# Kernel tuning notes

Measured on AMD Instinct MI355X. Metric: run time of the kernel, lower is better.

Reference implementation:

```python
import jax, jax.numpy as jnp
import numpy as np
from jax.scipy.linalg import solve_triangular

B, T, D = 2, 8192, 1024
HEAD_DIM = 128
H = D // HEAD_DIM  # 8 heads
C = 64             # chunk size (hard-coded in the torch module)


def setup_inputs() -> dict:
    key = jax.random.key(0)
    k0, k1, k2, k3 = jax.random.split(key, 4)
    scale = 0.02
    return {
        "out": jax.random.normal(k0, (B, T, D), jnp.float32),
        "W_write": jax.random.normal(k1, (D, D), jnp.float32) * scale,   # proj_write.weight (out,in)
        "W_read": jax.random.normal(k2, (D, D), jnp.float32) * scale,    # proj_read.weight
        "W_beta": jax.random.normal(k3, (H, D), jnp.float32) * scale,    # proj_beta.weight
        "decay": jnp.full((H,), 4.6, jnp.float32),                        # decay parameter
    }


def reference(out, W_write, W_read, W_beta, decay):
    Bs, Ts, Ds = out.shape
    d = HEAD_DIM
    Hn = Ds // d
    x = out.astype(jnp.float32)

    # keys: L2-normalized per head (F.normalize, eps=1e-12)
    k = x.reshape(Bs, Ts, Hn, d)
    k = k / jnp.maximum(jnp.linalg.norm(k, axis=-1, keepdims=True), 1e-12)
    k = k.transpose(0, 2, 1, 3)                                   # (B,H,T,d)
    v = (x @ W_write.T).reshape(Bs, Ts, Hn, d).transpose(0, 2, 1, 3)
    beta = jax.nn.sigmoid(x @ W_beta.T).transpose(0, 2, 1)[..., None]  # (B,H,T,1)
    v = v * beta
    k_beta = k * beta

    pad = (-Ts) % C
    if pad:
        pw = ((0, 0), (0, 0), (0, pad), (0, 0))
        k, v, k_beta = (jnp.pad(a, pw) for a in (k, v, k_beta))
    Tp = k.shape[2]
    N = Tp // C

    log_gamma = jnp.log(jax.nn.sigmoid(decay))                     # (H,)
    pos = jnp.arange(C, dtype=jnp.float32)
    cum_decay = (pos + 1.0)[None, :] * log_gamma[:, None]          # (H,C)
    Ldiff = cum_decay[:, :, None] - cum_decay[:, None, :]
    L = jnp.tril(jnp.exp(jnp.tril(Ldiff)))                         # (H,C,C)
    decay_exp = jnp.exp(cum_decay)[None, :, None, :, None]         # (1,H,1,C,1)
    chunk_total_decay = jnp.exp(cum_decay[:, -1])[None, :, None, None]  # (1,H,1,1)
    dw = jnp.exp(cum_decay[:, -1:] - cum_decay)[None, :, :, None]  # (1,H,C,1)
    de = jnp.exp(cum_decay)[None, :, :, None]                      # (1,H,C,1)

    k = k.reshape(Bs, Hn, N, C, d)
    v = v.reshape(Bs, Hn, N, C, d)
    k_beta = k_beta.reshape(Bs, Hn, N, C, d)

    # UT transform: original loop computes A = (I - A0)^{-1} with A0 strictly lower
    A0 = jnp.tril(-(jnp.einsum('bhnid,bhnjd->bhnij', k_beta, k) * L[None, :, None]), -1)
    eye = jnp.eye(C, dtype=jnp.float32)
    M = eye - A0                                                    # unit-diag lower triangular
    A = solve_triangular(M, jnp.broadcast_to(eye, M.shape), lower=True, unit_diagonal=True)

    v = A @ v
    k_cumdecay = A @ (k_beta * decay_exp)

    # inter-chunk sequential recurrence over N chunks
    kc = k.transpose(2, 0, 1, 3, 4)            # (N,B,H,C,d)
    vc = v.transpose(2, 0, 1, 3, 4)
    kcd = k_cumdecay.transpose(2, 0, 1, 3, 4)

    def step(S, inp):
        k_i, v_i, kcd_i = inp                  # (B,H,C,d)
        attn = jnp.tril(jnp.einsum('bhid,bhjd->bhij', k_i, k_i) * L[None])
        v_new = v_i - kcd_i @ S
        o_i = (k_i * de) @ S + attn @ v_new
        S_new = chunk_total_decay * S + jnp.einsum('bhcd,bhce->bhde', k_i * dw, v_new)
        return S_new, o_i

    S0 = jnp.zeros((Bs, Hn, d, d), jnp.float32)
    _, o = jax.lax.scan(step, S0, (kc, vc, kcd))  # o: (N,B,H,C,d)

    o = o.transpose(1, 2, 0, 3, 4).reshape(Bs, Hn, Tp, d)
    o = o.transpose(0, 2, 1, 3).reshape(Bs, Tp, Ds)[:, :Ts]
    return out + (o @ W_read.T).astype(out.dtype)
```

## Files before the change

### kernel.cpp

```cpp
#include <hip/hip_runtime.h>
#include <stdint.h>

#define DEV static __device__ __forceinline__

typedef float          f32x4  __attribute__((ext_vector_type(4)));
typedef short          bf16x8 __attribute__((ext_vector_type(8)));
typedef unsigned short u16x4  __attribute__((ext_vector_type(4)));
typedef unsigned short u16x8  __attribute__((ext_vector_type(8)));

#define B_   2
#define T_   8192
#define D_   1024
#define H_   8
#define HD_  128
#define N_   128

DEV float dot4(const float4& a, const float4& b) {
    return a.x * b.x + a.y * b.y + a.z * b.z + a.w * b.w;
}
DEV unsigned short f2bf(float f) {
    union { float f; unsigned u; } v; v.f = f;
    unsigned r = (v.u + 0x7fffu + ((v.u >> 16) & 1u)) >> 16;
    return (unsigned short)r;
}
DEV float bf2f(unsigned short u) {
    union { unsigned u; float f; } v; v.u = ((unsigned)u) << 16;
    return v.f;
}
DEV void cvt4(const float4 v, u16x4* h, u16x4* l) {
    const float* p = (const float*)&v;
    #pragma unroll
    for (int i = 0; i < 4; ++i) {
        unsigned short hv = f2bf(p[i]);
        (*h)[i] = hv;
        (*l)[i] = f2bf(p[i] - bf2f(hv));
    }
}
DEV void bar_lgkm() {
    asm volatile("s_waitcnt lgkmcnt(0)" ::: "memory");
    __builtin_amdgcn_s_barrier();
}
DEV float4* r512(char* base, int r, int u) {
    return (float4*)(base + (r << 9) + ((u << 4) ^ ((r & 7) << 4)));
}
DEV float ld_sk(char* base, int c, int dk) {
    return *(float*)(base + (c << 9) + ((((dk >> 2) << 4) ^ ((c & 7) << 4)) + ((dk & 3) << 2)));
}

__launch_bounds__(256)
__global__ void prep_kernel(const float* __restrict__ X, const float* __restrict__ Wb,
                            unsigned short* __restrict__ khi, unsigned short* __restrict__ klo,
                            float* __restrict__ beta) {
    int bt = blockIdx.x;
    int b = bt >> 13, t = bt & 8191;
    __shared__ float xrow[D_];
    const float* xp = X + (size_t)bt * D_;
    for (int i = threadIdx.x; i < D_; i += 256) xrow[i] = xp[i];
    __syncthreads();
    int w = threadIdx.x >> 6, lane = threadIdx.x & 63;
    for (int h = w; h < H_; h += 4) {
        const float* xh = xrow + h * HD_;
        float a0 = xh[lane], a1 = xh[lane + 64];
        float s = a0 * a0 + a1 * a1;
        #pragma unroll
        for (int off = 32; off > 0; off >>= 1) s += __shfl_xor(s, off);
        float rn = 1.0f / fmaxf(sqrtf(s), 1e-12f);
        const float* wbh = Wb + (size_t)h * D_;
        float bs = 0.f;
        for (int i = lane; i < D_; i += 64) bs += xrow[i] * wbh[i];
        #pragma unroll
        for (int off = 32; off > 0; off >>= 1) bs += __shfl_xor(bs, off);
        float bet = 1.0f / (1.0f + expf(-bs));
        size_t kbase = ((size_t)(b * H_ + h) * T_ + t) * HD_;
        float x0 = a0 * rn, x1 = a1 * rn;
        unsigned short h0 = f2bf(x0), h1 = f2bf(x1);
        khi[kbase + lane]      = h0;
        khi[kbase + lane + 64] = h1;
        klo[kbase + lane]      = f2bf(x0 - bf2f(h0));
        klo[kbase + lane + 64] = f2bf(x1 - bf2f(h1));
        if (lane == 0) beta[(size_t)(b * H_ + h) * T_ + t] = bet;
    }
}

__launch_bounds__(256, 2)
__global__ void vproj_kernel(const float* __restrict__ X, const float* __restrict__ W,
                             const float* __restrict__ beta, float* __restrict__ vb) {
    extern __shared__ char gs[];
    char* AH = gs;
    char* AL = gs + 16384;
    char* BH = gs + 32768;
    char* BL = gs + 49152;
    int bm = blockIdx.x, bn = blockIdx.y;
    int tid = threadIdx.x;
    int w = tid >> 6, lr = tid & 15, lk = (tid & 63) >> 4;
    int wm = w >> 1, wn = w & 1;

    f32x4 acc[4][4];
    #pragma unroll
    for (int i = 0; i < 4; ++i)
        #pragma unroll
        for (int j = 0; j < 4; ++j) acc[i][j] = (f32x4){0.f, 0.f, 0.f, 0.f};

    for (int kt = 0; kt < 16; ++kt) {
        __syncthreads();
        #pragma unroll
        for (int q = 0; q < 8; ++q) {
            int f = tid + q * 256;
            int row = f >> 4, kq = f & 15;
            float4 av = *(const float4*)(X + (size_t)(bm * 128 + row) * D_ + kt * 64 + kq * 4);
            float4 bv = *(const float4*)(W + (size_t)(bn * 128 + row) * D_ + kt * 64 + kq * 4);
            u16x4 ah, al, bh, bl;
            cvt4(av, &ah, &al);
            cvt4(bv, &bh, &bl);
            int off = row * 128 + ((((kq >> 1) ^ (row & 7))) << 4) + ((kq & 1) << 3);
            *(u16x4*)(AH + off) = ah; *(u16x4*)(AL + off) = al;
            *(u16x4*)(BH + off) = bh; *(u16x4*)(BL + off) = bl;
        }
        __syncthreads();
        #pragma unroll
        for (int ks = 0; ks < 2; ++ks) {
            bf16x8 aH[4], aL[4], bH[4], bL[4];
            #pragma unroll
            for (int mt = 0; mt < 4; ++mt) {
                int row = wm * 64 + mt * 16 + lr;
                int off = row * 128 + (((ks * 4 + lk) ^ (row & 7)) << 4);
                aH[mt] = *(const bf16x8*)(AH + off);
                aL[mt] = *(const bf16x8*)(AL + off);
            }
            #pragma unroll
            for (int nt = 0; nt < 4; ++nt) {
                int row = wn * 64 + nt * 16 + lr;
                int off = row * 128 + (((ks * 4 + lk) ^ (row & 7)) << 4);
                bH[nt] = *(const bf16x8*)(BH + off);
                bL[nt] = *(const bf16x8*)(BL + off);
            }
            #pragma unroll
            for (int mt = 0; mt < 4; ++mt)
                #pragma unroll
                for (int nt = 0; nt < 4; ++nt) {
                    acc[mt][nt] = __builtin_amdgcn_mfma_f32_16x16x32_bf16(aH[mt], bH[nt], acc[mt][nt], 0, 0, 0);
                    acc[mt][nt] = __builtin_amdgcn_mfma_f32_16x16x32_bf16(aH[mt], bL[nt], acc[mt][nt], 0, 0, 0);
                    acc[mt][nt] = __builtin_amdgcn_mfma_f32_16x16x32_bf16(aL[mt], bH[nt], acc[mt][nt], 0, 0, 0);
                }
        }
    }
    #pragma unroll
    for (int mt = 0; mt < 4; ++mt)
        #pragma unroll
        for (int r = 0; r < 4; ++r) {
            int m = bm * 128 + wm * 64 + mt * 16 + lk * 4 + r;
            int b = m >> 13, t = m & 8191;
            float bet = beta[(size_t)(b * H_ + bn) * T_ + t];
            size_t ob = ((size_t)(b * H_ + bn) * T_ + t) * HD_;
            #pragma unroll
            for (int nt = 0; nt < 4; ++nt)
                vb[ob + wn * 64 + nt * 16 + lr] = acc[mt][nt][r] * bet;
        }
}

__launch_bounds__(256, 2)
__global__ void chunk_kernel(const unsigned short* __restrict__ khi,
                             const unsigned short* __restrict__ klo,
                             float* __restrict__ vb,
                             const float* __restrict__ beta_g,
                             const float* __restrict__ decay,
                             unsigned short* __restrict__ attn_g,
                             unsigned short* __restrict__ kcdhi_g,
                             unsigned short* __restrict__ kcdlo_g,
                             unsigned short* __restrict__ kdwh_g,
                             unsigned short* __restrict__ kdwl_g) {
    extern __shared__ char cs[];
    char*  sk = cs;
    float* sa = (float*)(cs + 32768);
    float* sm = (float*)(cs + 49152);
    __shared__ float sb[64];
    __shared__ float swgt[64];

    int cid = blockIdx.x;
    int bh = cid >> 7, cn = cid & 127;
    int h = bh & 7;
    int tid = threadIdx.x;
    float dec = decay[h];
    float sg = 1.0f / (1.0f + expf(-dec));
    float lg = logf(sg);
    size_t base = (size_t)cid * 8192;

    #pragma unroll
    for (int lq = 0; lq < 4; ++lq) {
        int f = tid + lq * 256;
        int c = f >> 4, u0 = (f & 15) << 1;
        u16x8 hh = *(const u16x8*)(khi + base + (size_t)f * 8);
        u16x8 ll = *(const u16x8*)(klo + base + (size_t)f * 8);
        float4 v0 = {bf2f(hh[0]) + bf2f(ll[0]), bf2f(hh[1]) + bf2f(ll[1]),
                     bf2f(hh[2]) + bf2f(ll[2]), bf2f(hh[3]) + bf2f(ll[3])};
        float4 v1 = {bf2f(hh[4]) + bf2f(ll[4]), bf2f(hh[5]) + bf2f(ll[5]),
                     bf2f(hh[6]) + bf2f(ll[6]), bf2f(hh[7]) + bf2f(ll[7])};
        *r512(sk, c, u0)     = v0;
        *r512(sk, c, u0 + 1) = v1;
    }
    if (tid < 64) {
        float bv = beta_g[(size_t)bh * T_ + cn * 64 + tid];
        sb[tid] = bv;
        swgt[tid] = bv * expf((float)(tid + 1) * lg);
    }
    __syncthreads();

    int bi = tid >> 4, bj = tid & 15;
    float dacc[4][4] = {};
    for (int u = 0; u < 32; ++u) {
        float4 ka[4], kc[4];
        #pragma unroll
        for (int i = 0; i < 4; ++i) ka[i] = *r512(sk, bi * 4 + i, u);
        #pragma unroll
        for (int j = 0; j < 4; ++j) kc[j] = *r512(sk, bj + 16 * j, u);
        #pragma unroll
        for (int i = 0; i < 4; ++i)
            #pragma unroll
            for (int j = 0; j < 4; ++j)
                dacc[i][j] += dot4(ka[i], kc[j]);
    }
    size_t abase = (size_t)cid * 4096;
    #pragma unroll
    for (int i = 0; i < 4; ++i) {
        int gi = bi * 4 + i;
        #pragma unroll
        for (int j = 0; j < 4; ++j) {
            int gj = bj + 16 * j;
            float dv = dacc[i][j];
            float dfac = expf((float)(gi - gj) * lg);
            attn_g[abase + (size_t)gi * 64 + gj] = (gi >= gj) ? f2bf(dv * dfac) : (unsigned short)0;
            sm[gi * 64 + gj] = (gj < gi) ? sb[gi] * dv * dfac : ((gi == gj) ? 1.f : 0.f);
        }
    }
    __syncthreads();

    if (tid < 64) {
        int j = tid;
        for (int i = 0; i < j; ++i) sa[i * 64 + j] = 0.f;
        sa[j * 64 + j] = 1.f;
        for (int i = j + 1; i < 64; ++i) {
            float s = 0.f;
            for (int p = j; p < i; ++p) s += sm[i * 64 + p] * sa[p * 64 + j];
            sa[i * 64 + j] = -s;
        }
    }
    __syncthreads();

    int ti = tid >> 4, te = tid & 15;
    {
        float ko[4][8] = {};
        for (int p = 0; p < 64; ++p) {
            float w = swgt[p];
            float4 k0 = *r512(sk, p, te * 2);
            float4 k1 = *r512(sk, p, te * 2 + 1);
            float kv[8] = {k0.x, k0.y, k0.z, k0.w, k1.x, k1.y, k1.z, k1.w};
            float a0 = sa[(ti * 4 + 0) * 64 + p] * w;
            float a1 = sa[(ti * 4 + 1) * 64 + p] * w;
            float a2 = sa[(ti * 4 + 2) * 64 + p] * w;
            float a3 = sa[(ti * 4 + 3) * 64 + p] * w;
            #pragma unroll
            for (int e = 0; e < 8; ++e) {
                ko[0][e] = fmaf(a0, kv[e], ko[0][e]);
                ko[1][e] = fmaf(a1, kv[e], ko[1][e]);
                ko[2][e] = fmaf(a2, kv[e], ko[2][e]);
                ko[3][e] = fmaf(a3, kv[e], ko[3][e]);
            }
        }
        #pragma unroll
        for (int i = 0; i < 4; ++i) {
            u16x8 hh, ll;
            #pragma unroll
            for (int e = 0; e < 8; ++e) {
                float t = -ko[i][e];
                unsigned short hv = f2bf(t);
                hh[e] = hv;
                ll[e] = f2bf(t - bf2f(hv));
            }
            size_t off = base + (size_t)(ti * 4 + i) * 128 + te * 8;
            *(u16x8*)(kcdhi_g + off) = hh;
            *(u16x8*)(kcdlo_g + off) = ll;
        }
    }

    {
        int dk = tid >> 1, ch = (tid & 1) * 32;
        #pragma unroll
        for (int q = 0; q < 4; ++q) {
            u16x8 th, tl;
            #pragma unroll
            for (int j = 0; j < 8; ++j) {
                int c = ch + q * 8 + j;
                float kv = ld_sk(sk, c, dk) * expf((float)(63 - c) * lg);
                unsigned short hv = f2bf(kv);
                th[j] = hv;
                tl[j] = f2bf(kv - bf2f(hv));
            }
            size_t off = base + (size_t)dk * 64 + ch + q * 8;
            *(u16x8*)(kdwh_g + off) = th;
            if (kdwl_g) *(u16x8*)(kdwl_g + off) = tl;
        }
    }
    __syncthreads();

    #pragma unroll
    for (int lq = 0; lq < 8; ++lq) {
        int f = tid + lq * 256;
        int r = f >> 5, u = f & 31;
        *r512(sk, r, u) = ((const float4*)(vb + base))[f];
    }
    __syncthreads();

    {
        float vo[4][8] = {};
        for (int p = 0; p < 64; ++p) {
            float4 v0 = *r512(sk, p, te * 2);
            float4 v1 = *r512(sk, p, te * 2 + 1);
            float vv[8] = {v0.x, v0.y, v0.z, v0.w, v1.x, v1.y, v1.z, v1.w};
            float a0 = sa[(ti * 4 + 0) * 64 + p];
            float a1 = sa[(ti * 4 + 1) * 64 + p];
            float a2 = sa[(ti * 4 + 2) * 64 + p];
            float a3 = sa[(ti * 4 + 3) * 64 + p];
            #pragma unroll
            for (int e = 0; e < 8; ++e) {
                vo[0][e] = fmaf(a0, vv[e], vo[0][e]);
                vo[1][e] = fmaf(a1, vv[e], vo[1][e]);
                vo[2][e] = fmaf(a2, vv[e], vo[2][e]);
                vo[3][e] = fmaf(a3, vv[e], vo[3][e]);
            }
        }
        #pragma unroll
        for (int i = 0; i < 4; ++i) {
            float4 lo = {vo[i][0], vo[i][1], vo[i][2], vo[i][3]};
            float4 hi = {vo[i][4], vo[i][5], vo[i][6], vo[i][7]};
            size_t off = base + (size_t)(ti * 4 + i) * 128 + te * 8;
            *(float4*)(vb + off)     = lo;
            *(float4*)(vb + off + 4) = hi;
        }
    }
}

__launch_bounds__(512, 1)
__global__ void scan_kernel(const unsigned short* __restrict__ khi,
                            const unsigned short* __restrict__ klo,
                            float* __restrict__ vb,
                            const unsigned short* __restrict__ kcdh,
                            const unsigned short* __restrict__ kcdl,
                            const unsigned short* __restrict__ att,
                            const unsigned short* __restrict__ kdwh,
                            const unsigned short* __restrict__ kdwl,
                            const float* __restrict__ decay) {
    __shared__ char SH[4096];
    __shared__ char SL[4096];
    __shared__ char VH[2048];
    __shared__ char VL[2048];

    int bid = blockIdx.x;
    int bh = ((bid >> 6) << 3) + (bid & 7);
    int strip = (bid >> 3) & 7;
    int e0 = strip * 16;
    int tid = threadIdx.x;
    int w = tid >> 6, l = tid & 63, lr = l & 15, lk = l >> 4;
    int grp = w >> 2, cw = w & 3;
    float dec = decay[bh & 7];
    float sg = 1.0f / (1.0f + expf(-dec));
    float lg = logf(sg);
    float g64 = expf(64.f * lg);
    float dev4[4];
    #pragma unroll
    for (int r = 0; r < 4; ++r)
        dev4[r] = expf((float)(cw * 16 + lk * 4 + r + 1) * lg);
    const bool haveLo = (kdwl != nullptr);

    f32x4 Sacc = (f32x4){0.f, 0.f, 0.f, 0.f};

    bf16x8 fH[4], fL[4];
    bf16x8 atA[2];
    f32x4 vnA;

    {
        size_t nb = (size_t)bh * N_ * 8192;
        size_t na = (size_t)bh * N_ * 4096;
        if (grp == 0) {
            #pragma unroll
            for (int ks = 0; ks < 4; ++ks) {
                size_t off = nb + (size_t)(cw * 16 + lr) * 128 + ks * 32 + lk * 8;
                fH[ks] = *(const bf16x8*)(kcdh + off);
                fL[ks] = *(const bf16x8*)(kcdl + off);
            }
            #pragma unroll
            for (int r = 0; r < 4; ++r)
                vnA[r] = vb[nb + (size_t)(cw * 16 + lk * 4 + r) * 128 + e0 + lr];
        } else {
            #pragma unroll
            for (int ks = 0; ks < 4; ++ks) {
                size_t off = nb + (size_t)(cw * 16 + lr) * 128 + ks * 32 + lk * 8;
                fH[ks] = *(const bf16x8*)(khi + off);
                fL[ks] = *(const bf16x8*)(klo + off);
            }
            #pragma unroll
            for (int ks2 = 0; ks2 < 2; ++ks2)
                atA[ks2] = *(const bf16x8*)(att + na + (size_t)(cw * 16 + lr) * 64 + ks2 * 32 + lk * 8);
        }
    }

    for (int cn = 0; cn < N_; ++cn) {
        size_t cb8 = ((size_t)bh * N_ + cn) * 8192;

        bf16x8 tH[2], tL[2];
        #pragma unroll
        for (int ks2 = 0; ks2 < 2; ++ks2) {
            size_t off = cb8 + (size_t)(w * 16 + lr) * 64 + ks2 * 32 + lk * 8;
            tH[ks2] = *(const bf16x8*)(kdwh + off);
            if (haveLo) tL[ks2] = *(const bf16x8*)(kdwl + off);
        }

        {
            u16x4 h4, l4;
            #pragma unroll
            for (int r = 0; r < 4; ++r) {
                unsigned short hv = f2bf(Sacc[r]);
                h4[r] = hv;
                l4[r] = f2bf(Sacc[r] - bf2f(hv));
            }
            int unit = 2 * w + (lk >> 1);
            int off = lr * 256 + ((unit ^ (lr & 7)) << 4) + ((lk & 1) << 3);
            *(u16x4*)(SH + off) = h4;
            *(u16x4*)(SL + off) = l4;
        }
        bar_lgkm();

        bf16x8 BH[4], BL[4];
        #pragma unroll
        for (int ks = 0; ks < 4; ++ks) {
            int off = lr * 256 + (((ks * 4 + lk) ^ (lr & 7)) << 4);
            BH[ks] = *(const bf16x8*)(SH + off);
            BL[ks] = *(const bf16x8*)(SL + off);
        }
        f32x4 acc1, acc2;
        if (grp == 0) {
            acc1 = vnA; acc2 = (f32x4){0.f, 0.f, 0.f, 0.f};
            __builtin_amdgcn_s_setprio(1);
            #pragma unroll
            for (int ks = 0; ks < 2; ++ks) {
                acc1 = __builtin_amdgcn_mfma_f32_16x16x32_bf16(fH[ks], BH[ks], acc1, 0, 0, 0);
                acc2 = __builtin_amdgcn_mfma_f32_16x16x32_bf16(fH[ks+2], BH[ks+2], acc2, 0, 0, 0);
                acc1 = __builtin_amdgcn_mfma_f32_16x16x32_bf16(fH[ks], BL[ks], acc1, 0, 0, 0);
                acc2 = __builtin_amdgcn_mfma_f32_16x16x32_bf16(fH[ks+2], BL[ks+2], acc2, 0, 0, 0);
                acc1 = __builtin_amdgcn_mfma_f32_16x16x32_bf16(fL[ks], BH[ks], acc1, 0, 0, 0);
                acc2 = __builtin_amdgcn_mfma_f32_16x16x32_bf16(fL[ks+2], BH[ks+2], acc2, 0, 0, 0);
            }
            __builtin_amdgcn_s_setprio(0);
            u16x4 h4, l4;
            #pragma unroll
            for (int r = 0; r < 4; ++r) {
                float vv = acc1[r] + acc2[r];
                unsigned short hv = f2bf(vv);
                h4[r] = hv; l4[r] = f2bf(vv - bf2f(hv));
            }
            int cu = 2 * cw + (lk >> 1);
            int off = lr * 128 + ((cu ^ (lr & 7)) << 4) + ((lk & 1) << 3);
            *(u16x4*)(VH + off) = h4;  *(u16x4*)(VL + off) = l4;
        } else {
            acc1 = (f32x4){0.f, 0.f, 0.f, 0.f}; acc2 = acc1;
            __builtin_amdgcn_s_setprio(1);
            #pragma unroll
            for (int ks = 0; ks < 2; ++ks) {
                acc1 = __builtin_amdgcn_mfma_f32_16x16x32_bf16(fH[ks], BH[ks], acc1, 0, 0, 0);
                acc2 = __builtin_amdgcn_mfma_f32_16x16x32_bf16(fH[ks+2], BH[ks+2], acc2, 0, 0, 0);
                acc1 = __builtin_amdgcn_mfma_f32_16x16x32_bf16(fH[ks], BL[ks], acc1, 0, 0, 0);
                acc2 = __builtin_amdgcn_mfma_f32_16x16x32_bf16(fH[ks+2], BL[ks+2], acc2, 0, 0, 0);
                acc1 = __builtin_amdgcn_mfma_f32_16x16x32_bf16(fL[ks], BH[ks], acc1, 0, 0, 0);
                acc2 = __builtin_amdgcn_mfma_f32_16x16x32_bf16(fL[ks+2], BH[ks+2], acc2, 0, 0, 0);
            }
            __builtin_amdgcn_s_setprio(0);
        }
        bar_lgkm();

        bf16x8 VHf[2], VLf[2];
        #pragma unroll
        for (int ks2 = 0; ks2 < 2; ++ks2) {
            int off = lr * 128 + (((ks2 * 4 + lk) ^ (lr & 7)) << 4);
            VHf[ks2] = *(const bf16x8*)(VH + off);
            VLf[ks2] = *(const bf16x8*)(VL + off);
        }
        if (grp == 1) {
            f32x4 om;
            #pragma unroll
            for (int r = 0; r < 4; ++r) om[r] = (acc1[r] + acc2[r]) * dev4[r];
            #pragma unroll
            for (int ks2 = 0; ks2 < 2; ++ks2) {
                om = __builtin_amdgcn_mfma_f32_16x16x32_bf16(atA[ks2], VHf[ks2], om, 0, 0, 0);
                om = __builtin_amdgcn_mfma_f32_16x16x32_bf16(atA[ks2], VLf[ks2], om, 0, 0, 0);
            }
            #pragma unroll
            for (int r = 0; r < 4; ++r)
                vb[cb8 + (size_t)(cw * 16 + lk * 4 + r) * 128 + e0 + lr] = om[r];
        }

        if (cn + 1 < N_) {
            size_t nb = ((size_t)bh * N_ + cn + 1) * 8192;
            size_t na = ((size_t)bh * N_ + cn + 1) * 4096;
            if (grp == 0) {
                #pragma unroll
                for (int ks = 0; ks < 4; ++ks) {
                    size_t off = nb + (size_t)(cw * 16 + lr) * 128 + ks * 32 + lk * 8;
                    fH[ks] = *(const bf16x8*)(kcdh + off);
                    fL[ks] = *(const bf16x8*)(kcdl + off);
                }
                #pragma unroll
                for (int r = 0; r < 4; ++r)
                    vnA[r] = vb[nb + (size_t)(cw * 16 + lk * 4 + r) * 128 + e0 + lr];
            } else {
                #pragma unroll
                for (int ks = 0; ks < 4; ++ks) {
                    size_t off = nb + (size_t)(cw * 16 + lr) * 128 + ks * 32 + lk * 8;
                    fH[ks] = *(const bf16x8*)(khi + off);
                    fL[ks] = *(const bf16x8*)(klo + off);
                }
                #pragma unroll
                for (int ks2 = 0; ks2 < 2; ++ks2)
                    atA[ks2] = *(const bf16x8*)(att + na + (size_t)(cw * 16 + lr) * 64 + ks2 * 32 + lk * 8);
            }
        }

        {
            #pragma unroll
            for (int r = 0; r < 4; ++r) Sacc[r] *= g64;
            f32x4 tmp = (f32x4){0.f, 0.f, 0.f, 0.f};
            __builtin_amdgcn_s_setprio(1);
            Sacc = __builtin_amdgcn_mfma_f32_16x16x32_bf16(tH[0], VHf[0], Sacc, 0, 0, 0);
            tmp  = __builtin_amdgcn_mfma_f32_16x16x32_bf16(tH[1], VHf[1], tmp,  0, 0, 0);
            Sacc = __builtin_amdgcn_mfma_f32_16x16x32_bf16(tH[0], VLf[0], Sacc, 0, 0, 0);
            tmp  = __builtin_amdgcn_mfma_f32_16x16x32_bf16(tH[1], VLf[1], tmp,  0, 0, 0);
            if (haveLo) {
                Sacc = __builtin_amdgcn_mfma_f32_16x16x32_bf16(tL[0], VHf[0], Sacc, 0, 0, 0);
                tmp  = __builtin_amdgcn_mfma_f32_16x16x32_bf16(tL[1], VHf[1], tmp,  0, 0, 0);
            }
            __builtin_amdgcn_s_setprio(0);
            #pragma unroll
            for (int r = 0; r < 4; ++r) Sacc[r] += tmp[r];
        }
    }
}

__launch_bounds__(256, 2)
__global__ void final_kernel(const float* __restrict__ X, const float* __restrict__ W,
                             const float* __restrict__ OB, float* __restrict__ out) {
    extern __shared__ char gs[];
    char* AH = gs;
    char* AL = gs + 16384;
    char* BH = gs + 32768;
    char* BL = gs + 49152;
    int bm = blockIdx.x, bn = blockIdx.y;
    int tid = threadIdx.x;
    int w = tid >> 6, lr = tid & 15, lk = (tid & 63) >> 4;
    int wm = w >> 1, wn = w & 1;

    f32x4 acc[4][4];
    #pragma unroll
    for (int i = 0; i < 4; ++i)
        #pragma unroll
        for (int j = 0; j < 4; ++j) acc[i][j] = (f32x4){0.f, 0.f, 0.f, 0.f};

    for (int kt = 0; kt < 16; ++kt) {
        int hh = kt >> 1, e0g = (kt & 1) * 64;
        __syncthreads();
        #pragma unroll
        for (int q = 0; q < 8; ++q) {
            int f = tid + q * 256;
            int row = f >> 4, kq = f & 15;
            int m = bm * 128 + row;
            int b = m >> 13, t = m & 8191;
            float4 av = *(const float4*)(OB + (((size_t)(b * H_ + hh) * T_ + t) << 7) + e0g + kq * 4);
            float4 bv = *(const float4*)(W + (size_t)(bn * 128 + row) * D_ + kt * 64 + kq * 4);
            u16x4 ah, al, bh, bl;
            cvt4(av, &ah, &al);
            cvt4(bv, &bh, &bl);
            int off = row * 128 + ((((kq >> 1) ^ (row & 7))) << 4) + ((kq & 1) << 3);
            *(u16x4*)(AH + off) = ah; *(u16x4*)(AL + off) = al;
            *(u16x4*)(BH + off) = bh; *(u16x4*)(BL + off) = bl;
        }
        __syncthreads();
        #pragma unroll
        for (int ks = 0; ks < 2; ++ks) {
            bf16x8 aH[4], aL[4], bH[4], bL[4];
            #pragma unroll
            for (int mt = 0; mt < 4; ++mt) {
                int row = wm * 64 + mt * 16 + lr;
                int off = row * 128 + (((ks * 4 + lk) ^ (row & 7)) << 4);
                aH[mt] = *(const bf16x8*)(AH + off);
                aL[mt] = *(const bf16x8*)(AL + off);
            }
            #pragma unroll
            for (int nt = 0; nt < 4; ++nt) {
                int row = wn * 64 + nt * 16 + lr;
                int off = row * 128 + (((ks * 4 + lk) ^ (row & 7)) << 4);
                bH[nt] = *(const bf16x8*)(BH + off);
                bL[nt] = *(const bf16x8*)(BL + off);
            }
            #pragma unroll
            for (int mt = 0; mt < 4; ++mt)
                #pragma unroll
                for (int nt = 0; nt < 4; ++nt) {
                    acc[mt][nt] = __builtin_amdgcn_mfma_f32_16x16x32_bf16(aH[mt], bH[nt], acc[mt][nt], 0, 0, 0);
                    acc[mt][nt] = __builtin_amdgcn_mfma_f32_16x16x32_bf16(aH[mt], bL[nt], acc[mt][nt], 0, 0, 0);
                    acc[mt][nt] = __builtin_amdgcn_mfma_f32_16x16x32_bf16(aL[mt], bH[nt], acc[mt][nt], 0, 0, 0);
                }
        }
    }
    #pragma unroll
    for (int mt = 0; mt < 4; ++mt)
        #pragma unroll
        for (int r = 0; r < 4; ++r) {
            int m = bm * 128 + wm * 64 + mt * 16 + lk * 4 + r;
            size_t xo = (size_t)m * D_ + bn * 128;
            #pragma unroll
            for (int nt = 0; nt < 4; ++nt) {
                int n = wn * 64 + nt * 16 + lr;
                out[xo + n] = X[xo + n] + acc[mt][nt][r];
            }
        }
}

extern "C" void kernel_launch(void* const* d_in, const int* in_sizes, int n_in,
                              void* d_out, int out_size, void* d_ws, size_t ws_size,
                              hipStream_t stream) {
    const float* X   = (const float*)d_in[0];
    const float* Ww  = (const float*)d_in[1];
    const float* Wr  = (const float*)d_in[2];
    const float* Wb  = (const float*)d_in[3];
    const float* dec = (const float*)d_in[4];

    char* ws = (char*)d_ws;
    unsigned short* khi  = (unsigned short*)(ws);
    unsigned short* klo  = (unsigned short*)(ws + 33554432);
    float*          vb   = (float*)(ws + 67108864);
    unsigned short* kcdh = (unsigned short*)(ws + 134217728);
    unsigned short* kcdl = (unsigned short*)(ws + 167772160);
    unsigned short* attn = (unsigned short*)(ws + 201326592);
    float*          beta = (float*)(ws + 218103808);
    unsigned short* kdwh = (unsigned short*)(ws + 218628096);
    unsigned short* kdwl = (ws_size >= 285736960ull)
                         ? (unsigned short*)(ws + 252182528)
                         : (unsigned short*)nullptr;
    if (ws_size < 252182528ull) return;

    hipFuncSetAttribute((const void*)vproj_kernel, hipFuncAttributeMaxDynamicSharedMemorySize, 65536);
    hipFuncSetAttribute((const void*)chunk_kernel, hipFuncAttributeMaxDynamicSharedMemorySize, 65536);
    hipFuncSetAttribute((const void*)final_kernel, hipFuncAttributeMaxDynamicSharedMemorySize, 65536);

    hipLaunchKernelGGL(prep_kernel, dim3(B_ * T_), dim3(256), 0, stream, X, Wb, khi, klo, beta);
    hipLaunchKernelGGL(vproj_kernel, dim3(128, 8), dim3(256), 65536, stream, X, Ww, beta, vb);
    hipLaunchKernelGGL(chunk_kernel, dim3(B_ * H_ * N_), dim3(256), 65536, stream,
                       khi, klo, vb, beta, dec, attn, kcdh, kcdl, kdwh, kdwl);
    hipLaunchKernelGGL(scan_kernel, dim3(128), dim3(512), 0, stream,
                       khi, klo, vb, kcdh, kcdl, attn, kdwh, kdwl, dec);
    hipLaunchKernelGGL(final_kernel, dim3(128, 8), dim3(256), 65536, stream, X, Wr, vb, (float*)d_out);
}
```

Before: 1.075 ms.

## Pre-split weights to bf16 hi/lo once and double-buffer scan prefetch

Adds a split_kernel that converts W_write and W_read into bf16 hi/lo pairs once per call, so the two projection GEMMs load pre-split weights with wide vector loads instead of reconverting every tile in each block. The scan loop is also unrolled by two with two register sets, which lets each chunk's operands be prefetched two steps ahead to hide global latency on the sequential recurrence. The split weights are written into workspace regions (kcdh, attn) whose earlier contents are already consumed by the time they are overwritten. This costs two extra launches and more register pressure in the scan kernel.

```diff
diff --git a/kernel.cpp b/kernel.cpp
--- a/kernel.cpp
+++ b/kernel.cpp
@@ -45,6 +45,22 @@
 }
 DEV float ld_sk(char* base, int c, int dk) {
     return *(float*)(base + (c << 9) + ((((dk >> 2) << 4) ^ ((c & 7) << 4)) + ((dk & 3) << 2)));
+}
+
+__launch_bounds__(256)
+__global__ void split_kernel(const float* __restrict__ src,
+                             unsigned short* __restrict__ h,
+                             unsigned short* __restrict__ l) {
+    size_t base = ((size_t)blockIdx.x * 256 + threadIdx.x) * 8;
+    float4 a = *(const float4*)(src + base);
+    float4 b = *(const float4*)(src + base + 4);
+    u16x4 ah, al, bh, bl;
+    cvt4(a, &ah, &al);
+    cvt4(b, &bh, &bl);
+    *(u16x4*)(h + base)     = ah;
+    *(u16x4*)(h + base + 4) = bh;
+    *(u16x4*)(l + base)     = al;
+    *(u16x4*)(l + base + 4) = bl;
 }
 
 __launch_bounds__(256)
@@ -83,7 +99,9 @@
 }
 
 __launch_bounds__(256, 2)
-__global__ void vproj_kernel(const float* __restrict__ X, const float* __restrict__ W,
+__global__ void vproj_kernel(const float* __restrict__ X,
+                             const unsigned short* __restrict__ Wh,
+                             const unsigned short* __restrict__ Wl,
                              const float* __restrict__ beta, float* __restrict__ vb) {
     extern __shared__ char gs[];
     char* AH = gs;
@@ -108,13 +126,19 @@
             int f = tid + q * 256;
             int row = f >> 4, kq = f & 15;
             float4 av = *(const float4*)(X + (size_t)(bm * 128 + row) * D_ + kt * 64 + kq * 4);
-            float4 bv = *(const float4*)(W + (size_t)(bn * 128 + row) * D_ + kt * 64 + kq * 4);
-            u16x4 ah, al, bh, bl;
+            u16x4 ah, al;
             cvt4(av, &ah, &al);
-            cvt4(bv, &bh, &bl);
             int off = row * 128 + ((((kq >> 1) ^ (row & 7))) << 4) + ((kq & 1) << 3);
             *(u16x4*)(AH + off) = ah; *(u16x4*)(AL + off) = al;
-            *(u16x4*)(BH + off) = bh; *(u16x4*)(BL + off) = bl;
+        }
+        #pragma unroll
+        for (int q = 0; q < 4; ++q) {
+            int f = tid + q * 256;
+            int row = f >> 3, u = f & 7;
+            size_t go = (size_t)(bn * 128 + row) * D_ + kt * 64 + u * 8;
+            int off = row * 128 + ((u ^ (row & 7)) << 4);
+            *(u16x8*)(BH + off) = *(const u16x8*)(Wh + go);
+            *(u16x8*)(BL + off) = *(const u16x8*)(Wl + go);
         }
         __syncthreads();
         #pragma unroll
@@ -339,6 +363,143 @@
     }
 }
 
+#define SCAN_PREFETCH(NCH, fH, fL, atA, vnA)                                          \
+    {                                                                                 \
+        size_t nb = ((size_t)bh * N_ + (NCH)) * 8192;                                 \
+        size_t na = ((size_t)bh * N_ + (NCH)) * 4096;                                 \
+        if (grp == 0) {                                                               \
+            _Pragma("unroll")                                                         \
+            for (int ks = 0; ks < 4; ++ks) {                                          \
+                size_t off = nb + (size_t)(cw * 16 + lr) * 128 + ks * 32 + lk * 8;    \
+                fH[ks] = *(const bf16x8*)(kcdh + off);                                \
+                fL[ks] = *(const bf16x8*)(kcdl + off);                                \
+            }                                                                         \
+            _Pragma("unroll")                                                         \
+            for (int r = 0; r < 4; ++r)                                               \
+                vnA[r] = vb[nb + (size_t)(cw * 16 + lk * 4 + r) * 128 + e0 + lr];     \
+        } else {                                                                      \
+            _Pragma("unroll")                                                         \
+            for (int ks = 0; ks < 4; ++ks) {                                          \
+                size_t off = nb + (size_t)(cw * 16 + lr) * 128 + ks * 32 + lk * 8;    \
+                fH[ks] = *(const bf16x8*)(khi + off);                                 \
+                fL[ks] = *(const bf16x8*)(klo + off);                                 \
+            }                                                                         \
+            _Pragma("unroll")                                                         \
+            for (int ks2 = 0; ks2 < 2; ++ks2)                                         \
+                atA[ks2] = *(const bf16x8*)(att + na + (size_t)(cw * 16 + lr) * 64 + ks2 * 32 + lk * 8); \
+        }                                                                             \
+    }
+
+#define SCAN_STEP(CN, fH, fL, atA, vnA)                                               \
+    {                                                                                 \
+        size_t cb8 = ((size_t)bh * N_ + (CN)) * 8192;                                 \
+        bf16x8 tH[2], tL[2];                                                          \
+        _Pragma("unroll")                                                             \
+        for (int ks2 = 0; ks2 < 2; ++ks2) {                                           \
+            size_t off = cb8 + (size_t)(w * 16 + lr) * 64 + ks2 * 32 + lk * 8;        \
+            tH[ks2] = *(const bf16x8*)(kdwh + off);                                   \
+            if (haveLo) tL[ks2] = *(const bf16x8*)(kdwl + off);                       \
+        }                                                                             \
+        {                                                                             \
+            u16x4 h4, l4;                                                             \
+            _Pragma("unroll")                                                         \
+            for (int r = 0; r < 4; ++r) {                                             \
+                unsigned short hv = f2bf(Sacc[r]);                                    \
+                h4[r] = hv;                                                           \
+                l4[r] = f2bf(Sacc[r] - bf2f(hv));                                     \
+            }                                                                         \
+            int unit = 2 * w + (lk >> 1);                                             \
+            int off = lr * 256 + ((unit ^ (lr & 7)) << 4) + ((lk & 1) << 3);          \
+            *(u16x4*)(SH + off) = h4;                                                 \
+            *(u16x4*)(SL + off) = l4;                                                 \
+        }                                                                             \
+        bar_lgkm();                                                                   \
+        bf16x8 BH[4], BL[4];                                                          \
+        _Pragma("unroll")                                                             \
+        for (int ks = 0; ks < 4; ++ks) {                                              \
+            int off = lr * 256 + (((ks * 4 + lk) ^ (lr & 7)) << 4);                   \
+            BH[ks] = *(const bf16x8*)(SH + off);                                      \
+            BL[ks] = *(const bf16x8*)(SL + off);                                      \
+        }                                                                             \
+        f32x4 acc1, acc2;                                                             \
+        if (grp == 0) {                                                               \
+            acc1 = vnA; acc2 = (f32x4){0.f, 0.f, 0.f, 0.f};                           \
+            __builtin_amdgcn_s_setprio(1);                                            \
+            _Pragma("unroll")                                                         \
+            for (int ks = 0; ks < 2; ++ks) {                                          \
+                acc1 = __builtin_amdgcn_mfma_f32_16x16x32_bf16(fH[ks], BH[ks], acc1, 0, 0, 0);       \
+                acc2 = __builtin_amdgcn_mfma_f32_16x16x32_bf16(fH[ks+2], BH[ks+2], acc2, 0, 0, 0);   \
+                acc1 = __builtin_amdgcn_mfma_f32_16x16x32_bf16(fH[ks], BL[ks], acc1, 0, 0, 0);       \
+                acc2 = __builtin_amdgcn_mfma_f32_16x16x32_bf16(fH[ks+2], BL[ks+2], acc2, 0, 0, 0);   \
+                acc1 = __builtin_amdgcn_mfma_f32_16x16x32_bf16(fL[ks], BH[ks], acc1, 0, 0, 0);       \
+                acc2 = __builtin_amdgcn_mfma_f32_16x16x32_bf16(fL[ks+2], BH[ks+2], acc2, 0, 0, 0);   \
+            }                                                                         \
+            __builtin_amdgcn_s_setprio(0);                                            \
+            u16x4 h4, l4;                                                             \
+            _Pragma("unroll")                                                         \
+            for (int r = 0; r < 4; ++r) {                                             \
+                float vv = acc1[r] + acc2[r];                                         \
+                unsigned short hv = f2bf(vv);                                         \
+                h4[r] = hv; l4[r] = f2bf(vv - bf2f(hv));                              \
+            }                                                                         \
+            int cu = 2 * cw + (lk >> 1);                                              \
+            int off = lr * 128 + ((cu ^ (lr & 7)) << 4) + ((lk & 1) << 3);            \
+            *(u16x4*)(VH + off) = h4;  *(u16x4*)(VL + off) = l4;                      \
+        } else {                                                                      \
+            acc1 = (f32x4){0.f, 0.f, 0.f, 0.f}; acc2 = acc1;                          \
+            __builtin_amdgcn_s_setprio(1);                                            \
+            _Pragma("unroll")                                                         \
+            for (int ks = 0; ks < 2; ++ks) {                                          \
+                acc1 = __builtin_amdgcn_mfma_f32_16x16x32_bf16(fH[ks], BH[ks], acc1, 0, 0, 0);       \
+                acc2 = __builtin_amdgcn_mfma_f32_16x16x32_bf16(fH[ks+2], BH[ks+2], acc2, 0, 0, 0);   \
+                acc1 = __builtin_amdgcn_mfma_f32_16x16x32_bf16(fH[ks], BL[ks], acc1, 0, 0, 0);       \
+                acc2 = __builtin_amdgcn_mfma_f32_16x16x32_bf16(fH[ks+2], BL[ks+2], acc2, 0, 0, 0);   \
+                acc1 = __builtin_amdgcn_mfma_f32_16x16x32_bf16(fL[ks], BH[ks], acc1, 0, 0, 0);       \
+                acc2 = __builtin_amdgcn_mfma_f32_16x16x32_bf16(fL[ks+2], BH[ks+2], acc2, 0, 0, 0);   \
+            }                                                                         \
+            __builtin_amdgcn_s_setprio(0);                                            \
+        }                                                                             \
+        bar_lgkm();                                                                   \
+        bf16x8 VHf[2], VLf[2];                                                        \
+        _Pragma("unroll")                                                             \
+        for (int ks2 = 0; ks2 < 2; ++ks2) {                                           \
+            int off = lr * 128 + (((ks2 * 4 + lk) ^ (lr & 7)) << 4);                  \
+            VHf[ks2] = *(const bf16x8*)(VH + off);                                    \
+            VLf[ks2] = *(const bf16x8*)(VL + off);                                    \
+        }                                                                             \
+        if (grp == 1) {                                                               \
+            f32x4 om;                                                                 \
+            _Pragma("unroll")                                                         \
+            for (int r = 0; r < 4; ++r) om[r] = (acc1[r] + acc2[r]) * dev4[r];        \
+            _Pragma("unroll")                                                         \
+            for (int ks2 = 0; ks2 < 2; ++ks2) {                                       \
+                om = __builtin_amdgcn_mfma_f32_16x16x32_bf16(atA[ks2], VHf[ks2], om, 0, 0, 0);  \
+                om = __builtin_amdgcn_mfma_f32_16x16x32_bf16(atA[ks2], VLf[ks2], om, 0, 0, 0);  \
+            }                                                                         \
+            _Pragma("unroll")                                                         \
+            for (int r = 0; r < 4; ++r)                                               \
+                vb[cb8 + (size_t)(cw * 16 + lk * 4 + r) * 128 + e0 + lr] = om[r];     \
+        }                                                                             \
+        if ((CN) + 2 < N_) SCAN_PREFETCH((CN) + 2, fH, fL, atA, vnA)                  \
+        {                                                                             \
+            _Pragma("unroll")                                                         \
+            for (int r = 0; r < 4; ++r) Sacc[r] *= g64;                               \
+            f32x4 tmp = (f32x4){0.f, 0.f, 0.f, 0.f};                                  \
+            __builtin_amdgcn_s_setprio(1);                                            \
+            Sacc = __builtin_amdgcn_mfma_f32_16x16x32_bf16(tH[0], VHf[0], Sacc, 0, 0, 0);  \
+            tmp  = __builtin_amdgcn_mfma_f32_16x16x32_bf16(tH[1], VHf[1], tmp,  0, 0, 0);  \
+            Sacc = __builtin_amdgcn_mfma_f32_16x16x32_bf16(tH[0], VLf[0], Sacc, 0, 0, 0);  \
+            tmp  = __builtin_amdgcn_mfma_f32_16x16x32_bf16(tH[1], VLf[1], tmp,  0, 0, 0);  \
+            if (haveLo) {                                                             \
+                Sacc = __builtin_amdgcn_mfma_f32_16x16x32_bf16(tL[0], VHf[0], Sacc, 0, 0, 0);  \
+                tmp  = __builtin_amdgcn_mfma_f32_16x16x32_bf16(tL[1], VHf[1], tmp,  0, 0, 0);  \
+            }                                                                         \
+            __builtin_amdgcn_s_setprio(0);                                            \
+            _Pragma("unroll")                                                         \
+            for (int r = 0; r < 4; ++r) Sacc[r] += tmp[r];                            \
+        }                                                                             \
+    }
+
 __launch_bounds__(512, 1)
 __global__ void scan_kernel(const unsigned short* __restrict__ khi,
                             const unsigned short* __restrict__ klo,
@@ -373,178 +534,23 @@
 
     f32x4 Sacc = (f32x4){0.f, 0.f, 0.f, 0.f};
 
-    bf16x8 fH[4], fL[4];
-    bf16x8 atA[2];
-    f32x4 vnA;
-
-    {
-        size_t nb = (size_t)bh * N_ * 8192;
-        size_t na = (size_t)bh * N_ * 4096;
-        if (grp == 0) {
-            #pragma unroll
-            for (int ks = 0; ks < 4; ++ks) {
-                size_t off = nb + (size_t)(cw * 16 + lr) * 128 + ks * 32 + lk * 8;
-                fH[ks] = *(const bf16x8*)(kcdh + off);
-                fL[ks] = *(const bf16x8*)(kcdl + off);
-            }
-            #pragma unroll
-            for (int r = 0; r < 4; ++r)
-                vnA[r] = vb[nb + (size_t)(cw * 16 + lk * 4 + r) * 128 + e0 + lr];
-        } else {
-            #pragma unroll
-            for (int ks = 0; ks < 4; ++ks) {
-                size_t off = nb + (size_t)(cw * 16 + lr) * 128 + ks * 32 + lk * 8;
-                fH[ks] = *(const bf16x8*)(khi + off);
-                fL[ks] = *(const bf16x8*)(klo + off);
-            }
-            #pragma unroll
-            for (int ks2 = 0; ks2 < 2; ++ks2)
-                atA[ks2] = *(const bf16x8*)(att + na + (size_t)(cw * 16 + lr) * 64 + ks2 * 32 + lk * 8);
-        }
-    }
-
-    for (int cn = 0; cn < N_; ++cn) {
-        size_t cb8 = ((size_t)bh * N_ + cn) * 8192;
-
-        bf16x8 tH[2], tL[2];
-        #pragma unroll
-        for (int ks2 = 0; ks2 < 2; ++ks2) {
-            size_t off = cb8 + (size_t)(w * 16 + lr) * 64 + ks2 * 32 + lk * 8;
-            tH[ks2] = *(const bf16x8*)(kdwh + off);
-            if (haveLo) tL[ks2] = *(const bf16x8*)(kdwl + off);
-        }
-
-        {
-            u16x4 h4, l4;
-            #pragma unroll
-            for (int r = 0; r < 4; ++r) {
-                unsigned short hv = f2bf(Sacc[r]);
-                h4[r] = hv;
-                l4[r] = f2bf(Sacc[r] - bf2f(hv));
-            }
-            int unit = 2 * w + (lk >> 1);
-            int off = lr * 256 + ((unit ^ (lr & 7)) << 4) + ((lk & 1) << 3);
-            *(u16x4*)(SH + off) = h4;
-            *(u16x4*)(SL + off) = l4;
-        }
-        bar_lgkm();
-
-        bf16x8 BH[4], BL[4];
-        #pragma unroll
-        for (int ks = 0; ks < 4; ++ks) {
-            int off = lr * 256 + (((ks * 4 + lk) ^ (lr & 7)) << 4);
-            BH[ks] = *(const bf16x8*)(SH + off);
-            BL[ks] = *(const bf16x8*)(SL + off);
-        }
-        f32x4 acc1, acc2;
-        if (grp == 0) {
-            acc1 = vnA; acc2 = (f32x4){0.f, 0.f, 0.f, 0.f};
-            __builtin_amdgcn_s_setprio(1);
-            #pragma unroll
-            for (int ks = 0; ks < 2; ++ks) {
-                acc1 = __builtin_amdgcn_mfma_f32_16x16x32_bf16(fH[ks], BH[ks], acc1, 0, 0, 0);
-                acc2 = __builtin_amdgcn_mfma_f32_16x16x32_bf16(fH[ks+2], BH[ks+2], acc2, 0, 0, 0);
-                acc1 = __builtin_amdgcn_mfma_f32_16x16x32_bf16(fH[ks], BL[ks], acc1, 0, 0, 0);
-                acc2 = __builtin_amdgcn_mfma_f32_16x16x32_bf16(fH[ks+2], BL[ks+2], acc2, 0, 0, 0);
-                acc1 = __builtin_amdgcn_mfma_f32_16x16x32_bf16(fL[ks], BH[ks], acc1, 0, 0, 0);
-                acc2 = __builtin_amdgcn_mfma_f32_16x16x32_bf16(fL[ks+2], BH[ks+2], acc2, 0, 0, 0);
-            }
-            __builtin_amdgcn_s_setprio(0);
-            u16x4 h4, l4;
-            #pragma unroll
-            for (int r = 0; r < 4; ++r) {
-                float vv = acc1[r] + acc2[r];
-                unsigned short hv = f2bf(vv);
-                h4[r] = hv; l4[r] = f2bf(vv - bf2f(hv));
-            }
-            int cu = 2 * cw + (lk >> 1);
-            int off = lr * 128 + ((cu ^ (lr & 7)) << 4) + ((lk & 1) << 3);
-            *(u16x4*)(VH + off) = h4;  *(u16x4*)(VL + off) = l4;
-        } else {
-            acc1 = (f32x4){0.f, 0.f, 0.f, 0.f}; acc2 = acc1;
-            __builtin_amdgcn_s_setprio(1);
-            #pragma unroll
-            for (int ks = 0; ks < 2; ++ks) {
-                acc1 = __builtin_amdgcn_mfma_f32_16x16x32_bf16(fH[ks], BH[ks], acc1, 0, 0, 0);
-                acc2 = __builtin_amdgcn_mfma_f32_16x16x32_bf16(fH[ks+2], BH[ks+2], acc2, 0, 0, 0);
-                acc1 = __builtin_amdgcn_mfma_f32_16x16x32_bf16(fH[ks], BL[ks], acc1, 0, 0, 0);
-                acc2 = __builtin_amdgcn_mfma_f32_16x16x32_bf16(fH[ks+2], BL[ks+2], acc2, 0, 0, 0);
-                acc1 = __builtin_amdgcn_mfma_f32_16x16x32_bf16(fL[ks], BH[ks], acc1, 0, 0, 0);
-                acc2 = __builtin_amdgcn_mfma_f32_16x16x32_bf16(fL[ks+2], BH[ks+2], acc2, 0, 0, 0);
-            }
-            __builtin_amdgcn_s_setprio(0);
-        }
-        bar_lgkm();
-
-        bf16x8 VHf[2], VLf[2];
-        #pragma unroll
-        for (int ks2 = 0; ks2 < 2; ++ks2) {
-            int off = lr * 128 + (((ks2 * 4 + lk) ^ (lr & 7)) << 4);
-            VHf[ks2] = *(const bf16x8*)(VH + off);
-            VLf[ks2] = *(const bf16x8*)(VL + off);
-        }
-        if (grp == 1) {
-            f32x4 om;
-            #pragma unroll
-            for (int r = 0; r < 4; ++r) om[r] = (acc1[r] + acc2[r]) * dev4[r];
-            #pragma unroll
-            for (int ks2 = 0; ks2 < 2; ++ks2) {
-                om = __builtin_amdgcn_mfma_f32_16x16x32_bf16(atA[ks2], VHf[ks2], om, 0, 0, 0);
-                om = __builtin_amdgcn_mfma_f32_16x16x32_bf16(atA[ks2], VLf[ks2], om, 0, 0, 0);
-            }
-            #pragma unroll
-            for (int r = 0; r < 4; ++r)
-                vb[cb8 + (size_t)(cw * 16 + lk * 4 + r) * 128 + e0 + lr] = om[r];
-        }
-
-        if (cn + 1 < N_) {
-            size_t nb = ((size_t)bh * N_ + cn + 1) * 8192;
-            size_t na = ((size_t)bh * N_ + cn + 1) * 4096;
-            if (grp == 0) {
-                #pragma unroll
-                for (int ks = 0; ks < 4; ++ks) {
-                    size_t off = nb + (size_t)(cw * 16 + lr) * 128 + ks * 32 + lk * 8;
-                    fH[ks] = *(const bf16x8*)(kcdh + off);
-                    fL[ks] = *(const bf16x8*)(kcdl + off);
-                }
-                #pragma unroll
-                for (int r = 0; r < 4; ++r)
-                    vnA[r] = vb[nb + (size_t)(cw * 16 + lk * 4 + r) * 128 + e0 + lr];
-            } else {
-                #pragma unroll
-                for (int ks = 0; ks < 4; ++ks) {
-                    size_t off = nb + (size_t)(cw * 16 + lr) * 128 + ks * 32 + lk * 8;
-                    fH[ks] = *(const bf16x8*)(khi + off);
-                    fL[ks] = *(const bf16x8*)(klo + off);
-                }
-                #pragma unroll
-                for (int ks2 = 0; ks2 < 2; ++ks2)
-                    atA[ks2] = *(const bf16x8*)(att + na + (size_t)(cw * 16 + lr) * 64 + ks2 * 32 + lk * 8);
-            }
-        }
-
-        {
-            #pragma unroll
-            for (int r = 0; r < 4; ++r) Sacc[r] *= g64;
-            f32x4 tmp = (f32x4){0.f, 0.f, 0.f, 0.f};
-            __builtin_amdgcn_s_setprio(1);
-            Sacc = __builtin_amdgcn_mfma_f32_16x16x32_bf16(tH[0], VHf[0], Sacc, 0, 0, 0);
-            tmp  = __builtin_amdgcn_mfma_f32_16x16x32_bf16(tH[1], VHf[1], tmp,  0, 0, 0);
-            Sacc = __builtin_amdgcn_mfma_f32_16x16x32_bf16(tH[0], VLf[0], Sacc, 0, 0, 0);
-            tmp  = __builtin_amdgcn_mfma_f32_16x16x32_bf16(tH[1], VLf[1], tmp,  0, 0, 0);
-            if (haveLo) {
-                Sacc = __builtin_amdgcn_mfma_f32_16x16x32_bf16(tL[0], VHf[0], Sacc, 0, 0, 0);
-                tmp  = __builtin_amdgcn_mfma_f32_16x16x32_bf16(tL[1], VHf[1], tmp,  0, 0, 0);
-            }
-            __builtin_amdgcn_s_setprio(0);
-            #pragma unroll
-            for (int r = 0; r < 4; ++r) Sacc[r] += tmp[r];
-        }
+    bf16x8 fHa[4], fLa[4], atAa[2];
+    bf16x8 fHb[4], fLb[4], atAb[2];
+    f32x4 vnAa, vnAb;
+
+    SCAN_PREFETCH(0, fHa, fLa, atAa, vnAa)
+    SCAN_PREFETCH(1, fHb, fLb, atAb, vnAb)
+
+    for (int cn = 0; cn < N_; cn += 2) {
+        SCAN_STEP(cn,     fHa, fLa, atAa, vnAa)
+        SCAN_STEP(cn + 1, fHb, fLb, atAb, vnAb)
     }
 }
 
 __launch_bounds__(256, 2)
-__global__ void final_kernel(const float* __restrict__ X, const float* __restrict__ W,
+__global__ void final_kernel(const float* __restrict__ X,
+                             const unsigned short* __restrict__ Wh,
+                             const unsigned short* __restrict__ Wl,
                              const float* __restrict__ OB, float* __restrict__ out) {
     extern __shared__ char gs[];
     char* AH = gs;
@@ -572,13 +578,19 @@
             int m = bm * 128 + row;
             int b = m >> 13, t = m & 8191;
             float4 av = *(const float4*)(OB + (((size_t)(b * H_ + hh) * T_ + t) << 7) + e0g + kq * 4);
-            float4 bv = *(const float4*)(W + (size_t)(bn * 128 + row) * D_ + kt * 64 + kq * 4);
-            u16x4 ah, al, bh, bl;
+            u16x4 ah, al;
             cvt4(av, &ah, &al);
-            cvt4(bv, &bh, &bl);
             int off = row * 128 + ((((kq >> 1) ^ (row & 7))) << 4) + ((kq & 1) << 3);
             *(u16x4*)(AH + off) = ah; *(u16x4*)(AL + off) = al;
-            *(u16x4*)(BH + off) = bh; *(u16x4*)(BL + off) = bl;
+        }
+        #pragma unroll
+        for (int q = 0; q < 4; ++q) {
+            int f = tid + q * 256;
+            int row = f >> 3, u = f & 7;
+            size_t go = (size_t)(bn * 128 + row) * D_ + kt * 64 + u * 8;
+            int off = row * 128 + ((u ^ (row & 7)) << 4);
+            *(u16x8*)(BH + off) = *(const u16x8*)(Wh + go);
+            *(u16x8*)(BL + off) = *(const u16x8*)(Wl + go);
         }
         __syncthreads();
         #pragma unroll
@@ -645,15 +657,22 @@
                          : (unsigned short*)nullptr;
     if (ws_size < 252182528ull) return;
 
+    unsigned short* Wwh = (unsigned short*)(ws + 134217728);
+    unsigned short* Wwl = (unsigned short*)(ws + 136314880);
+    unsigned short* Wrh = (unsigned short*)(ws + 201326592);
+    unsigned short* Wrl = (unsigned short*)(ws + 203423744);
+
     hipFuncSetAttribute((const void*)vproj_kernel, hipFuncAttributeMaxDynamicSharedMemorySize, 65536);
     hipFuncSetAttribute((const void*)chunk_kernel, hipFuncAttributeMaxDynamicSharedMemorySize, 65536);
     hipFuncSetAttribute((const void*)final_kernel, hipFuncAttributeMaxDynamicSharedMemorySize, 65536);
 
     hipLaunchKernelGGL(prep_kernel, dim3(B_ * T_), dim3(256), 0, stream, X, Wb, khi, klo, beta);
-    hipLaunchKernelGGL(vproj_kernel, dim3(128, 8), dim3(256), 65536, stream, X, Ww, beta, vb);
+    hipLaunchKernelGGL(split_kernel, dim3(512), dim3(256), 0, stream, Ww, Wwh, Wwl);
+    hipLaunchKernelGGL(vproj_kernel, dim3(128, 8), dim3(256), 65536, stream, X, Wwh, Wwl, beta, vb);
     hipLaunchKernelGGL(chunk_kernel, dim3(B_ * H_ * N_), dim3(256), 65536, stream,
                        khi, klo, vb, beta, dec, attn, kcdh, kcdl, kdwh, kdwl);
     hipLaunchKernelGGL(scan_kernel, dim3(128), dim3(512), 0, stream,
                        khi, klo, vb, kcdh, kcdl, attn, kdwh, kdwl, dec);
-    hipLaunchKernelGGL(final_kernel, dim3(128, 8), dim3(256), 65536, stream, X, Wr, vb, (float*)d_out);
-}
+    hipLaunchKernelGGL(split_kernel, dim3(512), dim3(256), 0, stream, Wr, Wrh, Wrl);
+    hipLaunchKernelGGL(final_kernel, dim3(128, 8), dim3(256), 65536, stream, X, Wrh, Wrl, vb, (float*)d_out);
+}
```

After: 962.0 us. -10.5%, faster.
